# Kernel tuning notes

Measured on AMD Instinct MI355X. Metric: run time of the kernel, lower is better.

The kernel has to match this reference:

```python
import jax, jax.numpy as jnp
import numpy as np

B, S, DIM, H, DH = 2, 2048, 1024, 16, 64
EPS = 1e-6


def rms_norm(x, w):
    # x: (..., DH); computed in fp32 like the torch module
    norm = jax.lax.rsqrt(jnp.mean(jnp.square(x), axis=-1, keepdims=True) + EPS)
    return (x * norm) * w


def apply_rope(x, freqs):
    # x: (B, H, S, D), freqs: (S, D); torch code slices cos/sin to first half
    d = x.shape[-1] // 2
    cos = jnp.cos(freqs)[None, None, :, :d]
    sin = jnp.sin(freqs)[None, None, :, :d]
    x1, x2 = x[..., :d], x[..., d:]
    return jnp.concatenate([x1 * cos - x2 * sin, x2 * cos + x1 * sin], axis=-1)


def setup_inputs() -> dict:
    key = jax.random.key(0)
    ks = jax.random.split(key, 4)
    x = jax.random.normal(ks[0], (B, S, DIM), dtype=jnp.float32)
    # causal additive mask
    causal = jnp.tril(jnp.ones((S, S), dtype=bool))
    mask = jnp.where(causal, 0.0, -1e9).astype(jnp.float32)[None, None]
    # standard rope frequencies: pos * inv_freq over head_dim
    inv_freq = 1.0 / (10000.0 ** (jnp.arange(0, DH, dtype=jnp.float32) / DH))
    rope_freqs = jnp.arange(S, dtype=jnp.float32)[:, None] * inv_freq[None, :]
    total = H * DH
    w_qkv = jax.random.normal(ks[1], (3 * total, DIM), dtype=jnp.float32) * (DIM ** -0.5)
    w_out = jax.random.normal(ks[2], (DIM, total), dtype=jnp.float32) * (total ** -0.5)
    q_norm_w = jnp.ones((DH,), dtype=jnp.float32)
    k_norm_w = jnp.ones((DH,), dtype=jnp.float32)
    return {"x": x, "mask": mask, "rope_freqs": rope_freqs, "w_qkv": w_qkv,
            "w_out": w_out, "q_norm_w": q_norm_w, "k_norm_w": k_norm_w}


def reference(x, mask, rope_freqs, w_qkv, w_out, q_norm_w, k_norm_w):
    b, s, _ = x.shape
    qkv = (x @ w_qkv.T).reshape(b, s, 3, H, DH)
    q, k, v = qkv[:, :, 0], qkv[:, :, 1], qkv[:, :, 2]
    q = jnp.transpose(rms_norm(q, q_norm_w), (0, 2, 1, 3))  # (B,H,S,DH)
    k = jnp.transpose(rms_norm(k, k_norm_w), (0, 2, 1, 3))
    v = jnp.transpose(v, (0, 2, 1, 3))
    q = apply_rope(q, rope_freqs)
    k = apply_rope(k, rope_freqs)
    scale = DH ** -0.5
    attn = jnp.einsum('bhsd,bhtd->bhst', q, k) * scale + mask
    attn = jax.nn.softmax(attn, axis=-1)
    out = jnp.einsum('bhst,bhtd->bhsd', attn, v)
    out = jnp.transpose(out, (0, 2, 1, 3)).reshape(b, s, H * DH)
    return out @ w_out.T
```

## Files before the change

kernel.cpp:

```cpp
#include <hip/hip_runtime.h>
#include <hip/hip_bf16.h>
#include <stdint.h>

typedef short bf16x8 __attribute__((ext_vector_type(8)));
typedef float f32x4  __attribute__((ext_vector_type(4)));

#define MFMA_BF16(a,b,c) __builtin_amdgcn_mfma_f32_16x16x32_bf16((a),(b),(c),0,0,0)

__device__ __forceinline__ void async_ld16(const void* g, void* l) {
  __builtin_amdgcn_global_load_lds(
      (const __attribute__((address_space(1))) void*)g,
      (__attribute__((address_space(3))) void*)l, 16, 0, 0);
}

__device__ __forceinline__ unsigned short bf16_bits(float x) {
  __hip_bfloat16 h = __float2bfloat16(x);
  return *(unsigned short*)&h;
}

#define NX_C    (2 * 2048 * 1024)
#define NWQKV_C (3072 * 1024)
#define NWOUT_C (1024 * 1024)

__global__ void __launch_bounds__(256)
cvt_all(const float* __restrict__ x, const float* __restrict__ wqkv,
        const float* __restrict__ wout, __hip_bfloat16* __restrict__ dst)
{
  const int i = (blockIdx.x * 256 + threadIdx.x) * 4;
  const float* src;
  int off;
  if (i < NX_C)                { src = x;    off = i; }
  else if (i < NX_C + NWQKV_C) { src = wqkv; off = i - NX_C; }
  else                         { src = wout; off = i - NX_C - NWQKV_C; }
  const float4 v = *(const float4*)(src + off);
  ushort4 u;
  u.x = bf16_bits(v.x); u.y = bf16_bits(v.y);
  u.z = bf16_bits(v.z); u.w = bf16_bits(v.w);
  *(ushort4*)((unsigned short*)dst + i) = u;
}

template<int EPI>
__global__ void __launch_bounds__(256)
gemm_bt(const __hip_bfloat16* __restrict__ A,
        const __hip_bfloat16* __restrict__ B,
        int K,
        __hip_bfloat16* __restrict__ o0,
        __hip_bfloat16* __restrict__ o1,
        __hip_bfloat16* __restrict__ o2,
        float* __restrict__ of,
        const float* __restrict__ freqs,
        const float* __restrict__ qw,
        const float* __restrict__ kw)
{
  __shared__ __align__(16) __hip_bfloat16 As[2][128 * 32];
  __shared__ __align__(16) __hip_bfloat16 Bs[2][128 * 32];

  const int tid  = threadIdx.x;
  const int w    = tid >> 6;
  const int lane = tid & 63;
  const int quad = lane >> 4;
  const int l15  = lane & 15;

  const int m0 = blockIdx.y * 128;
  const int n0 = blockIdx.x * 128;

  const int srow = lane >> 2;
  const int sgr  = ((lane & 3) ^ ((lane >> 3) & 3)) * 8;
  const int c0 = w * 2, c1 = w * 2 + 1;

  const int pg = l15 * 32 + (quad ^ ((l15 >> 1) & 3)) * 8;

  const int wm = (w >> 1) * 64;
  const int wn = (w & 1) * 64;
  const int ac0 = (wm >> 4);
  const int bc0 = (wn >> 4);

  f32x4 acc[4][4] = {};

  async_ld16(A + (size_t)(m0 + c0 * 16 + srow) * K + sgr, &As[0][0] + c0 * 512);
  async_ld16(A + (size_t)(m0 + c1 * 16 + srow) * K + sgr, &As[0][0] + c1 * 512);
  async_ld16(B + (size_t)(n0 + c0 * 16 + srow) * K + sgr, &Bs[0][0] + c0 * 512);
  async_ld16(B + (size_t)(n0 + c1 * 16 + srow) * K + sgr, &Bs[0][0] + c1 * 512);

  const int niter = K >> 5;
  for (int it = 0; it < niter; ++it) {
    const int cur = it & 1;
    __syncthreads();
    if (it + 1 < niter) {
      const int kn = (it + 1) << 5;
      async_ld16(A + (size_t)(m0 + c0 * 16 + srow) * K + kn + sgr, &As[cur ^ 1][0] + c0 * 512);
      async_ld16(A + (size_t)(m0 + c1 * 16 + srow) * K + kn + sgr, &As[cur ^ 1][0] + c1 * 512);
      async_ld16(B + (size_t)(n0 + c0 * 16 + srow) * K + kn + sgr, &Bs[cur ^ 1][0] + c0 * 512);
      async_ld16(B + (size_t)(n0 + c1 * 16 + srow) * K + kn + sgr, &Bs[cur ^ 1][0] + c1 * 512);
    }

    const __hip_bfloat16* Ac = &As[cur][0];
    const __hip_bfloat16* Bc = &Bs[cur][0];
    bf16x8 af[4], bfr[4];
#pragma unroll
    for (int t = 0; t < 4; ++t) {
      af[t]  = *(const bf16x8*)(Ac + (ac0 + t) * 512 + pg);
      bfr[t] = *(const bf16x8*)(Bc + (bc0 + t) * 512 + pg);
    }
#pragma unroll
    for (int mt = 0; mt < 4; ++mt)
#pragma unroll
      for (int nt = 0; nt < 4; ++nt)
        acc[mt][nt] = MFMA_BF16(af[mt], bfr[nt], acc[mt][nt]);
  }

  if (EPI == 1) {
    const int ldc = (int)gridDim.x * 128;
#pragma unroll
    for (int mt = 0; mt < 4; ++mt)
#pragma unroll
      for (int nt = 0; nt < 4; ++nt)
#pragma unroll
        for (int r = 0; r < 4; ++r)
          of[(size_t)(m0 + wm + mt * 16 + quad * 4 + r) * ldc
             + n0 + wn + nt * 16 + l15] = acc[mt][nt][r];
    return;
  }

  const int which = n0 >> 10;
  const int hb    = ((n0 & 1023) >> 6) + (wn >> 6);

  if (which == 2) {
#pragma unroll
    for (int mt = 0; mt < 4; ++mt)
#pragma unroll
      for (int nt = 0; nt < 4; ++nt)
#pragma unroll
        for (int r = 0; r < 4; ++r) {
          const int m = m0 + wm + mt * 16 + quad * 4 + r;
          const int b = m >> 11, s = m & 2047;
          const int d = nt * 16 + l15;
          o2[((size_t)((b * 16 + hb) * 64 + d) << 11) + s] =
              __float2bfloat16(acc[mt][nt][r]);
        }
    return;
  }

  const float* wgt = which ? kw : qw;
  __hip_bfloat16* dst = which ? o1 : o0;
  const float wv0 = wgt[l15], wv1 = wgt[16 + l15];
  const float wv2 = wgt[32 + l15], wv3 = wgt[48 + l15];

#pragma unroll
  for (int mt = 0; mt < 4; ++mt) {
#pragma unroll
    for (int r = 0; r < 4; ++r) {
      float ssq = acc[mt][0][r] * acc[mt][0][r] + acc[mt][1][r] * acc[mt][1][r]
                + acc[mt][2][r] * acc[mt][2][r] + acc[mt][3][r] * acc[mt][3][r];
      ssq += __shfl_xor(ssq, 1);
      ssq += __shfl_xor(ssq, 2);
      ssq += __shfl_xor(ssq, 4);
      ssq += __shfl_xor(ssq, 8);
      float sc = rsqrtf(ssq * (1.0f / 64.0f) + 1e-6f);
      if (which == 0) sc *= 0.125f;

      const float y0 = acc[mt][0][r] * sc * wv0;
      const float y1 = acc[mt][1][r] * sc * wv1;
      const float y2 = acc[mt][2][r] * sc * wv2;
      const float y3 = acc[mt][3][r] * sc * wv3;

      const int m = m0 + wm + mt * 16 + quad * 4 + r;
      const int b = m >> 11, s = m & 2047;
      const float f0 = freqs[s * 64 + l15];
      const float f1 = freqs[s * 64 + 16 + l15];
      float sn0, cs0, sn1, cs1;
      __sincosf(f0, &sn0, &cs0);
      __sincosf(f1, &sn1, &cs1);

      const size_t row = ((size_t)((b * 16 + hb) * 2048 + s)) << 6;
      dst[row + l15]      = __float2bfloat16(y0 * cs0 - y2 * sn0);
      dst[row + 16 + l15] = __float2bfloat16(y1 * cs1 - y3 * sn1);
      dst[row + 32 + l15] = __float2bfloat16(y2 * cs0 + y0 * sn0);
      dst[row + 48 + l15] = __float2bfloat16(y3 * cs1 + y1 * sn1);
    }
  }
}

__global__ void __launch_bounds__(256, 2)
attn(const __hip_bfloat16* __restrict__ q,
     const __hip_bfloat16* __restrict__ k,
     const __hip_bfloat16* __restrict__ vt,
     __hip_bfloat16* __restrict__ ao)
{
  __shared__ __align__(16) __hip_bfloat16 Ks[2][64 * 64];
  __shared__ __align__(16) __hip_bfloat16 Vs[2][64 * 64];

  const int tid  = threadIdx.x;
  const int w    = tid >> 6;
  const int lane = tid & 63;
  const int quad = lane >> 4;
  const int l15  = lane & 15;

  const int lin  = blockIdx.x;
  const int c8   = lin & 7;
  const int rest = lin >> 3;
  const int pj   = rest & 15;
  const int bh   = ((rest >> 4) << 3) + c8;
  const int b    = bh >> 4, h = bh & 15;

  const __hip_bfloat16* qb = q  + (size_t)bh * 2048 * 64;
  const __hip_bfloat16* kb = k  + (size_t)bh * 2048 * 64;
  const __hip_bfloat16* vb = vt + (size_t)bh * 64 * 2048;

  const int pr = ((l15 >> 2) * 8) + (l15 & 3);

  const int pgk  = (quad ^ (l15 & 3) ^ (((l15 >> 2) & 1) << 2)) * 8;
  const int pgk4 = pgk ^ 32;
  const int pgv  = (quad ^ (l15 & 7)) * 8;
  const int pgv4 = pgv ^ 32;

  const int sj  = lane >> 3;
  const int sp  = lane & 7;
  const int kgA = (sp ^ (sj & 3)) * 8;
  const int kgB = kgA ^ 32;
  const int vgs = (sp ^ sj) * 8;
  const int ck0 = w * 2, ck1 = w * 2 + 1;

#define STAGE(KEY0, BUF) do {                                                     \
    __hip_bfloat16* ks_ = &Ks[BUF][0];                                            \
    __hip_bfloat16* vs_ = &Vs[BUF][0];                                            \
    async_ld16(kb + (size_t)((KEY0) + ck0 * 8 + sj) * 64 + kgA, ks_ + ck0 * 512); \
    async_ld16(kb + (size_t)((KEY0) + ck1 * 8 + sj) * 64 + kgB, ks_ + ck1 * 512); \
    async_ld16(vb + (size_t)(ck0 * 8 + sj) * 2048 + (KEY0) + vgs, vs_ + ck0 * 512); \
    async_ld16(vb + (size_t)(ck1 * 8 + sj) * 2048 + (KEY0) + vgs, vs_ + ck1 * 512); \
  } while (0)

  for (int pass = 0; pass < 2; ++pass) {
    const int J  = pass ? (31 - pj) : pj;
    const int q0 = J * 64 + w * 16;
    const int qi = q0 + l15;

    const bf16x8 bq0 = *(const bf16x8*)(qb + (size_t)qi * 64 + quad * 8);
    const bf16x8 bq1 = *(const bf16x8*)(qb + (size_t)qi * 64 + 32 + quad * 8);

    f32x4 o[4] = {};
    float lsum = 0.f;

    const int ntile = J + 1;

    __syncthreads();
    STAGE(0, 0);

    for (int kt = 0; kt < ntile; ++kt) {
      const int cur = kt & 1;
      const int t0 = kt * 64;

      __syncthreads();
      if (kt + 1 < ntile) STAGE(t0 + 64, cur ^ 1);

      const __hip_bfloat16* Kc = &Ks[cur][0];
      const __hip_bfloat16* Vc = &Vs[cur][0];

      bf16x8 ka00, ka01, ka10, ka11, kb00, kb01, kb10, kb11;
      ka00 = *(const bf16x8*)(Kc + (pr)      * 64 + pgk);
      ka01 = *(const bf16x8*)(Kc + (pr)      * 64 + pgk4);
      ka10 = *(const bf16x8*)(Kc + (pr + 4)  * 64 + pgk);
      ka11 = *(const bf16x8*)(Kc + (pr + 4)  * 64 + pgk4);
      kb00 = *(const bf16x8*)(Kc + (32 + pr)     * 64 + pgk);
      kb01 = *(const bf16x8*)(Kc + (32 + pr)     * 64 + pgk4);
      kb10 = *(const bf16x8*)(Kc + (32 + pr + 4) * 64 + pgk);
      kb11 = *(const bf16x8*)(Kc + (32 + pr + 4) * 64 + pgk4);

      bf16x8 va[2][4];
#pragma unroll
      for (int dt = 0; dt < 4; ++dt) {
        va[0][dt] = *(const bf16x8*)(Vc + (dt * 16 + l15) * 64 + pgv);
        va[1][dt] = *(const bf16x8*)(Vc + (dt * 16 + l15) * 64 + pgv4);
      }

      f32x4 c00 = {}, c01 = {}, c10 = {}, c11 = {};
      c00 = MFMA_BF16(ka00, bq0, c00); c00 = MFMA_BF16(ka01, bq1, c00);
      c01 = MFMA_BF16(ka10, bq0, c01); c01 = MFMA_BF16(ka11, bq1, c01);
      c10 = MFMA_BF16(kb00, bq0, c10); c10 = MFMA_BF16(kb01, bq1, c10);
      c11 = MFMA_BF16(kb10, bq0, c11); c11 = MFMA_BF16(kb11, bq1, c11);

      float e00[4], e01[4], e10[4], e11[4];
#pragma unroll
      for (int r = 0; r < 4; ++r) {
        e00[r] = c00[r]; e01[r] = c01[r]; e10[r] = c10[r]; e11[r] = c11[r];
      }

      if (kt == ntile - 1) {
#pragma unroll
        for (int r = 0; r < 4; ++r) {
          const int k0v = t0 + 8 * quad + r;
          if (k0v      > qi) e00[r] = -1e30f;
          if (k0v + 4  > qi) e01[r] = -1e30f;
          if (k0v + 32 > qi) e10[r] = -1e30f;
          if (k0v + 36 > qi) e11[r] = -1e30f;
        }
      }

      float rs = 0.f;
#pragma unroll
      for (int r = 0; r < 4; ++r) {
        e00[r] = __expf(e00[r] - 8.0f);
        e01[r] = __expf(e01[r] - 8.0f);
        e10[r] = __expf(e10[r] - 8.0f);
        e11[r] = __expf(e11[r] - 8.0f);
        rs += (e00[r] + e01[r]) + (e10[r] + e11[r]);
      }
      lsum += rs;

      bf16x8 pf0, pf1;
#pragma unroll
      for (int r = 0; r < 4; ++r) {
        pf0[r] = (short)bf16_bits(e00[r]);  pf0[r + 4] = (short)bf16_bits(e01[r]);
        pf1[r] = (short)bf16_bits(e10[r]);  pf1[r + 4] = (short)bf16_bits(e11[r]);
      }

#pragma unroll
      for (int dt = 0; dt < 4; ++dt) {
        o[dt] = MFMA_BF16(va[0][dt], pf0, o[dt]);
        o[dt] = MFMA_BF16(va[1][dt], pf1, o[dt]);
      }
    }

    lsum += __shfl_xor(lsum, 16);
    lsum += __shfl_xor(lsum, 32);

    const float inv = 1.0f / lsum;
    const size_t row = ((size_t)(b * 2048 + qi)) * 1024 + h * 64;
#pragma unroll
    for (int dt = 0; dt < 4; ++dt) {
      ushort4 u;
      u.x = bf16_bits(o[dt][0] * inv);
      u.y = bf16_bits(o[dt][1] * inv);
      u.z = bf16_bits(o[dt][2] * inv);
      u.w = bf16_bits(o[dt][3] * inv);
      *(ushort4*)((unsigned short*)ao + row + dt * 16 + quad * 4) = u;
    }
  }
#undef STAGE
}

extern "C" void kernel_launch(void* const* d_in, const int* in_sizes, int n_in,
                              void* d_out, int out_size, void* d_ws, size_t ws_size,
                              hipStream_t stream)
{
  const float* x    = (const float*)d_in[0];
  const float* rf   = (const float*)d_in[2];
  const float* wqkv = (const float*)d_in[3];
  const float* wout = (const float*)d_in[4];
  const float* qw   = (const float*)d_in[5];
  const float* kw   = (const float*)d_in[6];

  const size_t NE = (size_t)2 * 16 * 2048 * 64;

  __hip_bfloat16* qb  = (__hip_bfloat16*)d_ws;
  __hip_bfloat16* kb  = qb  + NE;
  __hip_bfloat16* vt  = kb  + NE;
  __hip_bfloat16* ao  = vt  + NE;
  __hip_bfloat16* xb  = ao  + NE;
  __hip_bfloat16* wqb = xb  + NX_C;
  __hip_bfloat16* wob = wqb + NWQKV_C;

  cvt_all<<<(NX_C + NWQKV_C + NWOUT_C) / 1024, 256, 0, stream>>>(x, wqkv, wout, xb);

  gemm_bt<0><<<dim3(24, 32), 256, 0, stream>>>(xb, wqb, 1024, qb, kb, vt,
                                               nullptr, rf, qw, kw);
  attn<<<512, 256, 0, stream>>>(qb, kb, vt, ao);
  gemm_bt<1><<<dim3(8, 32), 256, 0, stream>>>(ao, wob, 1024,
                                              nullptr, nullptr, nullptr, (float*)d_out,
                                              nullptr, nullptr, nullptr);
}
```

Baseline: 190.9 us.

## Triple-buffer GEMM LDS stages with two-ahead async prefetch and explicit vmcnt waits

The bf16 GEMM's shared-memory staging grows from two buffers to three. Loads are now issued two K-steps ahead, and each iteration uses a partial s_waitcnt vmcnt(4) plus a raw barrier instead of __syncthreads. This should hide more global-load latency behind the MFMA work. The cost is 50% more LDS per block, which may reduce occupancy, and correctness now depends on the hand-set vmcnt counts matching the four loads issued per stage.

```diff
diff --git a/kernel.cpp b/kernel.cpp
--- a/kernel.cpp
+++ b/kernel.cpp
@@ -52,8 +52,8 @@
         const float* __restrict__ qw,
         const float* __restrict__ kw)
 {
-  __shared__ __align__(16) __hip_bfloat16 As[2][128 * 32];
-  __shared__ __align__(16) __hip_bfloat16 Bs[2][128 * 32];
+  __shared__ __align__(16) __hip_bfloat16 As[3][128 * 32];
+  __shared__ __align__(16) __hip_bfloat16 Bs[3][128 * 32];
 
   const int tid  = threadIdx.x;
   const int w    = tid >> 6;
@@ -77,21 +77,34 @@
 
   f32x4 acc[4][4] = {};
 
-  async_ld16(A + (size_t)(m0 + c0 * 16 + srow) * K + sgr, &As[0][0] + c0 * 512);
-  async_ld16(A + (size_t)(m0 + c1 * 16 + srow) * K + sgr, &As[0][0] + c1 * 512);
-  async_ld16(B + (size_t)(n0 + c0 * 16 + srow) * K + sgr, &Bs[0][0] + c0 * 512);
-  async_ld16(B + (size_t)(n0 + c1 * 16 + srow) * K + sgr, &Bs[0][0] + c1 * 512);
+#define GSTAGE(KN, BUF) do {                                                        \
+    async_ld16(A + (size_t)(m0 + c0 * 16 + srow) * K + (KN) + sgr,                  \
+               &As[BUF][0] + c0 * 512);                                             \
+    async_ld16(A + (size_t)(m0 + c1 * 16 + srow) * K + (KN) + sgr,                  \
+               &As[BUF][0] + c1 * 512);                                             \
+    async_ld16(B + (size_t)(n0 + c0 * 16 + srow) * K + (KN) + sgr,                  \
+               &Bs[BUF][0] + c0 * 512);                                             \
+    async_ld16(B + (size_t)(n0 + c1 * 16 + srow) * K + (KN) + sgr,                  \
+               &Bs[BUF][0] + c1 * 512);                                             \
+  } while (0)
 
   const int niter = K >> 5;
+
+  GSTAGE(0, 0);
+  if (niter > 1) GSTAGE(32, 1);
+
+  int cur = 0;
   for (int it = 0; it < niter; ++it) {
-    const int cur = it & 1;
-    __syncthreads();
     if (it + 1 < niter) {
-      const int kn = (it + 1) << 5;
-      async_ld16(A + (size_t)(m0 + c0 * 16 + srow) * K + kn + sgr, &As[cur ^ 1][0] + c0 * 512);
-      async_ld16(A + (size_t)(m0 + c1 * 16 + srow) * K + kn + sgr, &As[cur ^ 1][0] + c1 * 512);
-      async_ld16(B + (size_t)(n0 + c0 * 16 + srow) * K + kn + sgr, &Bs[cur ^ 1][0] + c0 * 512);
-      async_ld16(B + (size_t)(n0 + c1 * 16 + srow) * K + kn + sgr, &Bs[cur ^ 1][0] + c1 * 512);
+      asm volatile("s_waitcnt vmcnt(4)" ::: "memory");
+    } else {
+      asm volatile("s_waitcnt vmcnt(0)" ::: "memory");
+    }
+    __builtin_amdgcn_s_barrier();
+
+    if (it + 2 < niter) {
+      int nb = cur + 2; if (nb >= 3) nb -= 3;
+      GSTAGE((it + 2) << 5, nb);
     }
 
     const __hip_bfloat16* Ac = &As[cur][0];
@@ -107,7 +120,10 @@
 #pragma unroll
       for (int nt = 0; nt < 4; ++nt)
         acc[mt][nt] = MFMA_BF16(af[mt], bfr[nt], acc[mt][nt]);
-  }
+
+    if (++cur == 3) cur = 0;
+  }
+#undef GSTAGE
 
   if (EPI == 1) {
     const int ldc = (int)gridDim.x * 128;
```

Result: no change. 192.2 us (+0.7%).
